# Optimization experiments

Measured on AMD Instinct MI355X. Metric: run time of the kernel, lower is better.

## Reference

```python
import jax, jax.numpy as jnp
import numpy as np

BS, C_IN, SEQ_LEN = 16, 321, 720
PRED_LEN, PATCH_LEN, STRIDE = 720, 24, 24
N_LAYERS, D_MODEL, N_HEADS, D_FF = 3, 128, 16, 256
SEQ_PN = (SEQ_LEN - PATCH_LEN) // STRIDE + 1   # 30
PRED_PN = (PRED_LEN + PATCH_LEN - 1) // PATCH_LEN  # 30
EPS = 1e-5


def layernorm(x, g, b):
    mu = x.mean(-1, keepdims=True)
    var = x.var(-1, keepdims=True)
    return (x - mu) * jax.lax.rsqrt(var + EPS) * g + b


def setup_inputs() -> dict:
    key = jax.random.key(0)
    ks = iter(jax.random.split(key, 32))
    w = lambda shape, s=0.02: jax.random.normal(next(ks), shape, jnp.float32) * s
    L = N_LAYERS
    return {
        "z": jax.random.normal(next(ks), (BS, C_IN, SEQ_LEN), jnp.float32),
        "W_P_w": w((D_MODEL, PATCH_LEN)), "W_P_b": jnp.zeros((D_MODEL,), jnp.float32),
        "PE": 0.04 * jax.random.uniform(next(ks), (SEQ_PN, D_MODEL), jnp.float32) - 0.02,
        "dummies": 0.5 * jax.random.normal(next(ks), (C_IN, PRED_PN, PATCH_LEN), jnp.float32),
        "Wq": w((L, D_MODEL, D_MODEL)), "bq": jnp.zeros((L, D_MODEL), jnp.float32),
        "Wk": w((L, D_MODEL, D_MODEL)), "bk": jnp.zeros((L, D_MODEL), jnp.float32),
        "Wv": w((L, D_MODEL, D_MODEL)), "bv": jnp.zeros((L, D_MODEL), jnp.float32),
        "Wo": w((L, D_MODEL, D_MODEL)), "bo": jnp.zeros((L, D_MODEL), jnp.float32),
        "g1": jnp.ones((L, D_MODEL), jnp.float32), "be1": jnp.zeros((L, D_MODEL), jnp.float32),
        "W1": w((L, D_FF, D_MODEL)), "b1": jnp.zeros((L, D_FF), jnp.float32),
        "W2": w((L, D_MODEL, D_FF // 2)), "b2": jnp.zeros((L, D_MODEL), jnp.float32),
        "g2": jnp.ones((L, D_MODEL), jnp.float32), "be2": jnp.zeros((L, D_MODEL), jnp.float32),
        "proj_w": w((PATCH_LEN, D_MODEL)), "proj_b": jnp.zeros((PATCH_LEN,), jnp.float32),
    }


def reference(z, W_P_w, W_P_b, PE, dummies, Wq, bq, Wk, bk, Wv, bv, Wo, bo,
              g1, be1, W1, b1, W2, b2, g2, be2, proj_w, proj_b):
    bs, c, _ = z.shape
    d_h = D_MODEL // N_HEADS
    scale = d_h ** -0.5
    # instance norm over time (unbiased=False var)
    mean = z.mean(2, keepdims=True)
    std = jnp.sqrt(z.var(2, keepdims=True) + EPS)
    zn = (z - mean) / std
    # unfold into patches: [bs, c, S, patch_len]
    idx = jnp.arange(SEQ_PN)[:, None] * STRIDE + jnp.arange(PATCH_LEN)[None, :]
    patches = zn[:, :, idx]
    x = jnp.einsum('bcsp,dp->bcsd', patches, W_P_w) + W_P_b + PE
    x = x.reshape(bs * c, SEQ_PN, D_MODEL)                       # seq tokens
    dum = jnp.einsum('cnp,dp->cnd', dummies, W_P_w) + W_P_b      # [c, Pn, d]
    pred = jnp.broadcast_to(dum[None], (bs, c, PRED_PN, D_MODEL)).reshape(bs * c, PRED_PN, D_MODEL)
    B = bs * c
    scores = None
    for i in range(N_LAYERS):
        q = (jnp.einsum('bpd,ed->bpe', pred, Wq[i]) + bq[i]).reshape(B, PRED_PN, N_HEADS, d_h)
        k = (jnp.einsum('bsd,ed->bse', x, Wk[i]) + bk[i]).reshape(B, SEQ_PN, N_HEADS, d_h)
        v = (jnp.einsum('bsd,ed->bse', x, Wv[i]) + bv[i]).reshape(B, SEQ_PN, N_HEADS, d_h)
        s = jnp.einsum('bphd,bshd->bphs', q, k) * scale
        if scores is not None:
            s = s + scores   # residual attention scores across layers
        scores = s
        attn = jax.nn.softmax(s, axis=-1)
        o = jnp.einsum('bphs,bshd->bphd', attn, v).reshape(B, PRED_PN, D_MODEL)
        o = jnp.einsum('bpd,ed->bpe', o, Wo[i]) + bo[i]
        pred = layernorm(pred + o, g1[i], be1[i])
        h = jnp.einsum('bpd,fd->bpf', pred, W1[i]) + b1[i]
        a, gate = jnp.split(h, 2, axis=-1)
        f = jnp.einsum('bpf,df->bpd', a * jax.nn.gelu(gate, approximate=False), W2[i]) + b2[i]
        pred = layernorm(pred + f, g2[i], be2[i])
    out = pred.reshape(bs, c, PRED_PN, D_MODEL)
    out = jnp.einsum('bcnd,pd->bcnp', out, proj_w) + proj_b
    out = out.reshape(bs, c, PRED_PN * PATCH_LEN)
    return out * std[:, :, 0:1] + mean[:, :, 0:1]
```

## Files before the change

### kernel.cpp

```cpp
#include <hip/hip_runtime.h>
#include <math.h>


typedef unsigned short u16;
typedef __attribute__((ext_vector_type(8))) short short8;
typedef __attribute__((ext_vector_type(4))) float floatx4;

#define ATTN_SCALE 0.35355339059327373f
#define SB 136
#define SF 132

#define MFMA_BF16 __builtin_amdgcn_mfma_f32_16x16x32_bf16

__device__ __forceinline__ u16 f2bf(float f){
  union{float f; unsigned u;} v; v.f=f;
  unsigned r = v.u + 0x7FFFu + ((v.u>>16)&1u);
  return (u16)(r>>16);
}
__device__ __forceinline__ float bf2f(u16 h){
  union{unsigned u; float f;} v; v.u = ((unsigned)h)<<16;
  return v.f;
}
__device__ __forceinline__ float gelu_f(float x){
  float u = x*(1.f + 0.044715f*x*x);
  float e = __expf(-1.5957691216057308f*u);
  return x/(1.f+e);
}

__device__ __forceinline__ short8 cvt8(const float* ap){
  floatx4 f0 = *(const floatx4*)ap;
  floatx4 f1 = *(const floatx4*)(ap+4);
  short8 a;
  a[0]=(short)f2bf(f0[0]); a[1]=(short)f2bf(f0[1]);
  a[2]=(short)f2bf(f0[2]); a[3]=(short)f2bf(f0[3]);
  a[4]=(short)f2bf(f1[0]); a[5]=(short)f2bf(f1[1]);
  a[6]=(short)f2bf(f1[2]); a[7]=(short)f2bf(f1[3]);
  return a;
}
__device__ __forceinline__ short8 loadB(const u16* p){ return *(const short8*)p; }
__device__ __forceinline__ short8 loadB(const float* p){ return cvt8(p); }

__device__ __forceinline__ void epi(u16* out, floatx4 acc, float bv, int rt, int qd, int col){
  #pragma unroll
  for (int r=0;r<4;++r){
    const int row = rt*16+qd*4+r;
    out[row*SB+col] = (row<30) ? f2bf(acc[r]+bv) : (u16)0;
  }
}

template<typename WT>
__device__ __forceinline__ void gemm2(const u16* A, const WT* __restrict__ W,
                                      const float* __restrict__ bias, u16* out,
                                      int wave, int lane){
  const int m=lane&15, qd=lane>>4, col=wave*16+m;
  floatx4 acc[2] = {{0.f,0.f,0.f,0.f},{0.f,0.f,0.f,0.f}};
  #pragma unroll
  for (int kt=0;kt<4;++kt){
    short8 b = loadB(W + col*128 + kt*32 + qd*8);
    #pragma unroll
    for (int rt=0;rt<2;++rt){
      short8 a = *(const short8*)(A + (rt*16+m)*SB + kt*32 + qd*8);
      acc[rt] = MFMA_BF16(a, b, acc[rt], 0,0,0);
    }
  }
  const float bv = bias[col];
  #pragma unroll
  for (int rt=0;rt<2;++rt) epi(out, acc[rt], bv, rt, qd, col);
}

template<typename WT>
__device__ __forceinline__ void gemm_kv(const u16* A,
                                        const WT* __restrict__ Wk, const float* __restrict__ bk,
                                        const WT* __restrict__ Wv, const float* __restrict__ bv_,
                                        u16* outk, u16* outv, int wave, int lane){
  const int m=lane&15, qd=lane>>4, col=wave*16+m;
  floatx4 acck[2] = {{0.f,0.f,0.f,0.f},{0.f,0.f,0.f,0.f}};
  floatx4 accv[2] = {{0.f,0.f,0.f,0.f},{0.f,0.f,0.f,0.f}};
  #pragma unroll
  for (int kt=0;kt<4;++kt){
    short8 bk8 = loadB(Wk + col*128 + kt*32 + qd*8);
    short8 bv8 = loadB(Wv + col*128 + kt*32 + qd*8);
    #pragma unroll
    for (int rt=0;rt<2;++rt){
      short8 a = *(const short8*)(A + (rt*16+m)*SB + kt*32 + qd*8);
      acck[rt] = MFMA_BF16(a, bk8, acck[rt], 0,0,0);
      accv[rt] = MFMA_BF16(a, bv8, accv[rt], 0,0,0);
    }
  }
  const float bkb = bk[col], bvb = bv_[col];
  #pragma unroll
  for (int rt=0;rt<2;++rt){
    epi(outk, acck[rt], bkb, rt, qd, col);
    epi(outv, accv[rt], bvb, rt, qd, col);
  }
}

template<typename WT>
__device__ __forceinline__ void gemm_h(const u16* A, const WT* __restrict__ W1,
                                       const float* __restrict__ b1, u16* out,
                                       int wave, int lane){
  const int m=lane&15, qd=lane>>4, col=wave*16+m;
  floatx4 acca[2] = {{0.f,0.f,0.f,0.f},{0.f,0.f,0.f,0.f}};
  floatx4 accg[2] = {{0.f,0.f,0.f,0.f},{0.f,0.f,0.f,0.f}};
  #pragma unroll
  for (int kt=0;kt<4;++kt){
    short8 ba = loadB(W1 + col*128 + kt*32 + qd*8);
    short8 bg = loadB(W1 + (128+col)*128 + kt*32 + qd*8);
    #pragma unroll
    for (int rt=0;rt<2;++rt){
      short8 a = *(const short8*)(A + (rt*16+m)*SB + kt*32 + qd*8);
      acca[rt] = MFMA_BF16(a, ba, acca[rt], 0,0,0);
      accg[rt] = MFMA_BF16(a, bg, accg[rt], 0,0,0);
    }
  }
  const float bab = b1[col], bgb = b1[128+col];
  #pragma unroll
  for (int rt=0;rt<2;++rt){
    #pragma unroll
    for (int r=0;r<4;++r){
      const int row = rt*16+qd*4+r;
      u16 res = 0;
      if (row<30){
        float a = acca[rt][r]+bab;
        float g = accg[rt][r]+bgb;
        res = f2bf(a * gelu_f(g));
      }
      out[row*SB+col] = res;
    }
  }
}

__device__ __forceinline__ void ln_res(float* pred, u16* predb, const u16* add,
                                       const float* __restrict__ g, const float* __restrict__ be,
                                       int wave, int lane){
  for (int rr=wave; rr<30; rr+=8){
    float* pr = pred + rr*SF;
    u16*  pbr = predb + rr*SB;
    const u16* ar = add + rr*SB;
    float v0 = pr[lane]    + bf2f(ar[lane]);
    float v1 = pr[lane+64] + bf2f(ar[lane+64]);
    float s = v0+v1, s2 = v0*v0+v1*v1;
    #pragma unroll
    for (int off=32; off>0; off>>=1){ s += __shfl_xor(s,off,64); s2 += __shfl_xor(s2,off,64); }
    float m = s*(1.f/128.f);
    float var = s2*(1.f/128.f) - m*m;
    float rstd = rsqrtf(var + 1e-5f);
    float o0 = (v0-m)*rstd*g[lane]    + be[lane];
    float o1 = (v1-m)*rstd*g[lane+64] + be[lane+64];
    pr[lane] = o0; pr[lane+64] = o1;
    pbr[lane] = f2bf(o0); pbr[lane+64] = f2bf(o1);
  }
}

__global__ void cvtw(const float* __restrict__ Wq, const float* __restrict__ Wk,
                     const float* __restrict__ Wv, const float* __restrict__ Wo,
                     const float* __restrict__ W1, const float* __restrict__ W2,
                     u16* __restrict__ ws){
  const int i = blockIdx.x*256 + threadIdx.x;
  float v;
  if      (i < 49152)  v = Wq[i];
  else if (i < 98304)  v = Wk[i-49152];
  else if (i < 147456) v = Wv[i-98304];
  else if (i < 196608) v = Wo[i-147456];
  else if (i < 294912) v = W1[i-196608];
  else                 v = W2[i-294912];
  ws[i] = f2bf(v);
}

template<typename WT>
__global__ void
__attribute__((amdgpu_flat_work_group_size(512,512), amdgpu_waves_per_eu(4)))
ts_fused(
  const float* __restrict__ z,    const float* __restrict__ WPw, const float* __restrict__ WPb,
  const float* __restrict__ PE,   const float* __restrict__ dums,
  const WT*    __restrict__ Wq_a, const float* __restrict__ bq_a,
  const WT*    __restrict__ Wk_a, const float* __restrict__ bk_a,
  const WT*    __restrict__ Wv_a, const float* __restrict__ bv_a,
  const WT*    __restrict__ Wo_a, const float* __restrict__ bo_a,
  const float* __restrict__ g1_a, const float* __restrict__ be1_a,
  const WT*    __restrict__ W1_a, const float* __restrict__ b1_a,
  const WT*    __restrict__ W2_a, const float* __restrict__ b2_a,
  const float* __restrict__ g2_a, const float* __restrict__ be2_a,
  const float* __restrict__ PJw,  const float* __restrict__ PJb,
  float* __restrict__ dout)
{
  __shared__ __align__(16) u16   x_s[32*SB];
  __shared__ __align__(16) u16   predb[32*SB];
  __shared__ __align__(16) float pred_s[30*SF];
  __shared__ __align__(16) u16   bufA[32*SB];
  __shared__ __align__(16) u16   bufB[32*SB];
  __shared__ __align__(16) u16   bufC[32*SB];
  __shared__ float redA[8], redB[8], stats[2];

  const int tid  = threadIdx.x;
  const int wave = tid >> 6;
  const int lane = tid & 63;
  const int bi   = blockIdx.x;
  const int c    = bi % 321;
  const float* zr = z + bi*720;

  float s=0.f, s2=0.f;
  for (int i=tid;i<720;i+=512){ float v=zr[i]; s+=v; s2+=v*v; }
  #pragma unroll
  for (int off=32; off>0; off>>=1){ s += __shfl_xor(s,off,64); s2 += __shfl_xor(s2,off,64); }
  if (lane==0){ redA[wave]=s; redB[wave]=s2; }
  __syncthreads();
  if (tid==0){
    float S=0.f,S2=0.f;
    #pragma unroll
    for (int w=0;w<8;++w){S+=redA[w];S2+=redB[w];}
    float mu = S*(1.f/720.f);
    float var = S2*(1.f/720.f) - mu*mu;
    stats[0]=mu; stats[1]=sqrtf(var+1e-5f);
  }
  __syncthreads();
  const float mu = stats[0], sd = stats[1], rsd = 1.f/sd;

  for (int i=tid;i<720;i+=512) bufA[i] = f2bf((zr[i]-mu)*rsd);
  __syncthreads();

  {
    const int m = lane&15, qd = lane>>4, col = wave*16+m;
    const short8 z8 = {0,0,0,0,0,0,0,0};
    short8 b = (qd<3) ? cvt8(WPw + col*24 + qd*8) : z8;
    const float bv = WPb[col];
    #pragma unroll
    for (int rt=0;rt<2;++rt){
      const int pm = rt*16+m;
      short8 ax = (pm<30 && qd<3) ? *(const short8*)(bufA + pm*24 + qd*8) : z8;
      short8 ap = (pm<30 && qd<3) ? cvt8(dums + c*720 + pm*24 + qd*8) : z8;
      floatx4 accx={0.f,0.f,0.f,0.f}, accp={0.f,0.f,0.f,0.f};
      accx = MFMA_BF16(ax,b,accx,0,0,0);
      accp = MFMA_BF16(ap,b,accp,0,0,0);
      #pragma unroll
      for (int r=0;r<4;++r){
        const int row = rt*16+qd*4+r;
        if (row<30){
          float pv = accp[r]+bv;
          x_s[row*SB+col]    = f2bf(accx[r]+bv+PE[row*128+col]);
          pred_s[row*SF+col] = pv;
          predb[row*SB+col]  = f2bf(pv);
        } else { x_s[row*SB+col]=0; predb[row*SB+col]=0; }
      }
    }
  }
  __syncthreads();

  float sc[30];
  #pragma unroll
  for (int i=0;i<30;++i) sc[i]=0.f;
  const int h = wave*2 + (lane>>5);
  const int p = lane & 31;

  for (int li=0; li<3; ++li){
    const WT* Wq = Wq_a + li*16384; const float* bq = bq_a + li*128;
    const WT* Wk = Wk_a + li*16384; const float* bk = bk_a + li*128;
    const WT* Wv = Wv_a + li*16384; const float* bv = bv_a + li*128;
    const WT* Wo = Wo_a + li*16384; const float* bo = bo_a + li*128;
    const WT* W1 = W1_a + li*32768; const float* b1 = b1_a + li*256;
    const WT* W2 = W2_a + li*16384; const float* b2 = b2_a + li*128;

    gemm2  (predb, Wq, bq, bufA, wave, lane);
    gemm_kv(x_s, Wk, bk, Wv, bv, bufB, bufC, wave, lane);
    __syncthreads();

    if (p < 30){
      short8 qq = *(const short8*)(bufA + p*SB + h*8);
      float qv[8];
      #pragma unroll
      for (int j=0;j<8;++j) qv[j]=bf2f((u16)qq[j]);
      #pragma unroll
      for (int si=0; si<30; ++si){
        short8 kk = *(const short8*)(bufB + si*SB + h*8);
        float d = 0.f;
        #pragma unroll
        for (int j=0;j<8;++j) d += qv[j]*bf2f((u16)kk[j]);
        sc[si] += d * ATTN_SCALE;
      }
      float mx = sc[0];
      #pragma unroll
      for (int si=1; si<30; ++si) mx = fmaxf(mx, sc[si]);
      float ssum = 0.f;
      float ov[8] = {0.f,0.f,0.f,0.f,0.f,0.f,0.f,0.f};
      #pragma unroll
      for (int si=0; si<30; ++si){
        float e = __expf(sc[si]-mx);
        ssum += e;
        short8 vv = *(const short8*)(bufC + si*SB + h*8);
        #pragma unroll
        for (int j=0;j<8;++j) ov[j] += e*bf2f((u16)vv[j]);
      }
      const float rn = 1.f/ssum;
      #pragma unroll
      for (int j=0;j<8;++j) bufA[p*SB+h*8+j] = f2bf(ov[j]*rn);
    }
    __syncthreads();

    gemm2(bufA, Wo, bo, bufB, wave, lane);
    __syncthreads();
    ln_res(pred_s, predb, bufB, g1_a+li*128, be1_a+li*128, wave, lane);
    __syncthreads();

    gemm_h(predb, W1, b1, bufC, wave, lane);
    __syncthreads();
    gemm2(bufC, W2, b2, bufB, wave, lane);
    __syncthreads();
    ln_res(pred_s, predb, bufB, g2_a+li*128, be2_a+li*128, wave, lane);
    __syncthreads();
  }

  {
    const int m = lane&15, qd = lane>>4;
    const short8 z8 = {0,0,0,0,0,0,0,0};
    float* orow = dout + bi*720;
    for (int t=wave; t<4; t+=8){
      const int rt=t>>1, ct=t&1;
      const int col = ct*16+m;
      floatx4 acc = {0.f,0.f,0.f,0.f};
      #pragma unroll
      for (int kt=0;kt<4;++kt){
        const int k0 = kt*32+qd*8;
        short8 a = *(const short8*)(predb + (rt*16+m)*SB + k0);
        short8 b = (col<24) ? cvt8(PJw + col*128 + k0) : z8;
        acc = MFMA_BF16(a,b,acc,0,0,0);
      }
      if (col<24){
        const float pb = PJb[col];
        #pragma unroll
        for (int r=0;r<4;++r){
          const int row = rt*16+qd*4+r;
          if (row<30) orow[row*24+col] = (acc[r]+pb)*sd + mu;
        }
      }
    }
  }
}

extern "C" void kernel_launch(void* const* d_in, const int* in_sizes, int n_in,
                              void* d_out, int out_size, void* d_ws, size_t ws_size,
                              hipStream_t stream) {
  (void)in_sizes; (void)n_in; (void)out_size;
  const float* z    = (const float*)d_in[0];
  const float* WPw  = (const float*)d_in[1];
  const float* WPb  = (const float*)d_in[2];
  const float* PE   = (const float*)d_in[3];
  const float* dums = (const float*)d_in[4];
  const float* Wq   = (const float*)d_in[5];
  const float* bq   = (const float*)d_in[6];
  const float* Wk   = (const float*)d_in[7];
  const float* bk   = (const float*)d_in[8];
  const float* Wv   = (const float*)d_in[9];
  const float* bv   = (const float*)d_in[10];
  const float* Wo   = (const float*)d_in[11];
  const float* bo   = (const float*)d_in[12];
  const float* g1   = (const float*)d_in[13];
  const float* be1  = (const float*)d_in[14];
  const float* W1   = (const float*)d_in[15];
  const float* b1   = (const float*)d_in[16];
  const float* W2   = (const float*)d_in[17];
  const float* b2   = (const float*)d_in[18];
  const float* g2   = (const float*)d_in[19];
  const float* be2  = (const float*)d_in[20];
  const float* PJw  = (const float*)d_in[21];
  const float* PJb  = (const float*)d_in[22];
  float* dout = (float*)d_out;

  const size_t need = (size_t)344064 * sizeof(u16);
  if (ws_size >= need){
    u16* ws = (u16*)d_ws;
    cvtw<<<dim3(1344), dim3(256), 0, stream>>>(Wq, Wk, Wv, Wo, W1, W2, ws);
    ts_fused<u16><<<dim3(5136), dim3(512), 0, stream>>>(
      z, WPw, WPb, PE, dums,
      ws,        bq, ws+49152,  bk, ws+98304, bv, ws+147456, bo,
      g1, be1, ws+196608, b1, ws+294912, b2, g2, be2, PJw, PJb, dout);
  } else {
    ts_fused<float><<<dim3(5136), dim3(512), 0, stream>>>(
      z, WPw, WPb, PE, dums,
      Wq, bq, Wk, bk, Wv, bv, Wo, bo,
      g1, be1, W1, b1, W2, b2, g2, be2, PJw, PJb, dout);
  }
}
```

Measured before the change: 1.029 ms.

## Halve block to 4 waves, double per-wave work, keep residual stream in registers

```diff
diff --git a/kernel.cpp b/kernel.cpp
--- a/kernel.cpp
+++ b/kernel.cpp
@@ -8,7 +8,7 @@
 
 #define ATTN_SCALE 0.35355339059327373f
 #define SB 136
-#define SF 132
+#define BUFSZ (30*SB)
 
 #define MFMA_BF16 __builtin_amdgcn_mfma_f32_16x16x32_bf16
 
@@ -44,7 +44,7 @@
   #pragma unroll
   for (int r=0;r<4;++r){
     const int row = rt*16+qd*4+r;
-    out[row*SB+col] = (row<30) ? f2bf(acc[r]+bv) : (u16)0;
+    if (row<30) out[row*SB+col] = f2bf(acc[r]+bv);
   }
 }
 
@@ -52,20 +52,27 @@
 __device__ __forceinline__ void gemm2(const u16* A, const WT* __restrict__ W,
                                       const float* __restrict__ bias, u16* out,
                                       int wave, int lane){
-  const int m=lane&15, qd=lane>>4, col=wave*16+m;
-  floatx4 acc[2] = {{0.f,0.f,0.f,0.f},{0.f,0.f,0.f,0.f}};
+  const int m=lane&15, qd=lane>>4, c0=wave*16+m;
+  floatx4 acc[2][2] = {{{0.f,0.f,0.f,0.f},{0.f,0.f,0.f,0.f}},
+                       {{0.f,0.f,0.f,0.f},{0.f,0.f,0.f,0.f}}};
   #pragma unroll
   for (int kt=0;kt<4;++kt){
-    short8 b = loadB(W + col*128 + kt*32 + qd*8);
+    short8 b0 = loadB(W + c0*128       + kt*32 + qd*8);
+    short8 b1 = loadB(W + (c0+64)*128  + kt*32 + qd*8);
     #pragma unroll
     for (int rt=0;rt<2;++rt){
       short8 a = *(const short8*)(A + (rt*16+m)*SB + kt*32 + qd*8);
-      acc[rt] = MFMA_BF16(a, b, acc[rt], 0,0,0);
-    }
-  }
-  const float bv = bias[col];
-  #pragma unroll
-  for (int rt=0;rt<2;++rt) epi(out, acc[rt], bv, rt, qd, col);
+      acc[0][rt] = MFMA_BF16(a, b0, acc[0][rt], 0,0,0);
+      acc[1][rt] = MFMA_BF16(a, b1, acc[1][rt], 0,0,0);
+    }
+  }
+  #pragma unroll
+  for (int ct=0;ct<2;++ct){
+    const int col = c0 + ct*64;
+    const float bv = bias[col];
+    #pragma unroll
+    for (int rt=0;rt<2;++rt) epi(out, acc[ct][rt], bv, rt, qd, col);
+  }
 }
 
 template<typename WT>
@@ -73,25 +80,35 @@
                                         const WT* __restrict__ Wk, const float* __restrict__ bk,
                                         const WT* __restrict__ Wv, const float* __restrict__ bv_,
                                         u16* outk, u16* outv, int wave, int lane){
-  const int m=lane&15, qd=lane>>4, col=wave*16+m;
-  floatx4 acck[2] = {{0.f,0.f,0.f,0.f},{0.f,0.f,0.f,0.f}};
-  floatx4 accv[2] = {{0.f,0.f,0.f,0.f},{0.f,0.f,0.f,0.f}};
+  const int m=lane&15, qd=lane>>4, c0=wave*16+m;
+  floatx4 acck[2][2] = {{{0.f,0.f,0.f,0.f},{0.f,0.f,0.f,0.f}},
+                        {{0.f,0.f,0.f,0.f},{0.f,0.f,0.f,0.f}}};
+  floatx4 accv[2][2] = {{{0.f,0.f,0.f,0.f},{0.f,0.f,0.f,0.f}},
+                        {{0.f,0.f,0.f,0.f},{0.f,0.f,0.f,0.f}}};
   #pragma unroll
   for (int kt=0;kt<4;++kt){
-    short8 bk8 = loadB(Wk + col*128 + kt*32 + qd*8);
-    short8 bv8 = loadB(Wv + col*128 + kt*32 + qd*8);
+    short8 bk0 = loadB(Wk + c0*128      + kt*32 + qd*8);
+    short8 bk1 = loadB(Wk + (c0+64)*128 + kt*32 + qd*8);
+    short8 bv0 = loadB(Wv + c0*128      + kt*32 + qd*8);
+    short8 bv1 = loadB(Wv + (c0+64)*128 + kt*32 + qd*8);
     #pragma unroll
     for (int rt=0;rt<2;++rt){
       short8 a = *(const short8*)(A + (rt*16+m)*SB + kt*32 + qd*8);
-      acck[rt] = MFMA_BF16(a, bk8, acck[rt], 0,0,0);
-      accv[rt] = MFMA_BF16(a, bv8, accv[rt], 0,0,0);
-    }
-  }
-  const float bkb = bk[col], bvb = bv_[col];
-  #pragma unroll
-  for (int rt=0;rt<2;++rt){
-    epi(outk, acck[rt], bkb, rt, qd, col);
-    epi(outv, accv[rt], bvb, rt, qd, col);
+      acck[0][rt] = MFMA_BF16(a, bk0, acck[0][rt], 0,0,0);
+      acck[1][rt] = MFMA_BF16(a, bk1, acck[1][rt], 0,0,0);
+      accv[0][rt] = MFMA_BF16(a, bv0, accv[0][rt], 0,0,0);
+      accv[1][rt] = MFMA_BF16(a, bv1, accv[1][rt], 0,0,0);
+    }
+  }
+  #pragma unroll
+  for (int ct=0;ct<2;++ct){
+    const int col = c0 + ct*64;
+    const float bkb = bk[col], bvb = bv_[col];
+    #pragma unroll
+    for (int rt=0;rt<2;++rt){
+      epi(outk, acck[ct][rt], bkb, rt, qd, col);
+      epi(outv, accv[ct][rt], bvb, rt, qd, col);
+    }
   }
 }
 
@@ -99,56 +116,67 @@
 __device__ __forceinline__ void gemm_h(const u16* A, const WT* __restrict__ W1,
                                        const float* __restrict__ b1, u16* out,
                                        int wave, int lane){
-  const int m=lane&15, qd=lane>>4, col=wave*16+m;
-  floatx4 acca[2] = {{0.f,0.f,0.f,0.f},{0.f,0.f,0.f,0.f}};
-  floatx4 accg[2] = {{0.f,0.f,0.f,0.f},{0.f,0.f,0.f,0.f}};
+  const int m=lane&15, qd=lane>>4, c0=wave*16+m;
+  floatx4 acca[2][2] = {{{0.f,0.f,0.f,0.f},{0.f,0.f,0.f,0.f}},
+                        {{0.f,0.f,0.f,0.f},{0.f,0.f,0.f,0.f}}};
+  floatx4 accg[2][2] = {{{0.f,0.f,0.f,0.f},{0.f,0.f,0.f,0.f}},
+                        {{0.f,0.f,0.f,0.f},{0.f,0.f,0.f,0.f}}};
   #pragma unroll
   for (int kt=0;kt<4;++kt){
-    short8 ba = loadB(W1 + col*128 + kt*32 + qd*8);
-    short8 bg = loadB(W1 + (128+col)*128 + kt*32 + qd*8);
+    short8 ba0 = loadB(W1 + c0*128        + kt*32 + qd*8);
+    short8 ba1 = loadB(W1 + (c0+64)*128   + kt*32 + qd*8);
+    short8 bg0 = loadB(W1 + (c0+128)*128  + kt*32 + qd*8);
+    short8 bg1 = loadB(W1 + (c0+192)*128  + kt*32 + qd*8);
     #pragma unroll
     for (int rt=0;rt<2;++rt){
       short8 a = *(const short8*)(A + (rt*16+m)*SB + kt*32 + qd*8);
-      acca[rt] = MFMA_BF16(a, ba, acca[rt], 0,0,0);
-      accg[rt] = MFMA_BF16(a, bg, accg[rt], 0,0,0);
-    }
-  }
-  const float bab = b1[col], bgb = b1[128+col];
-  #pragma unroll
-  for (int rt=0;rt<2;++rt){
-    #pragma unroll
-    for (int r=0;r<4;++r){
-      const int row = rt*16+qd*4+r;
-      u16 res = 0;
-      if (row<30){
-        float a = acca[rt][r]+bab;
-        float g = accg[rt][r]+bgb;
-        res = f2bf(a * gelu_f(g));
+      acca[0][rt] = MFMA_BF16(a, ba0, acca[0][rt], 0,0,0);
+      acca[1][rt] = MFMA_BF16(a, ba1, acca[1][rt], 0,0,0);
+      accg[0][rt] = MFMA_BF16(a, bg0, accg[0][rt], 0,0,0);
+      accg[1][rt] = MFMA_BF16(a, bg1, accg[1][rt], 0,0,0);
+    }
+  }
+  #pragma unroll
+  for (int ct=0;ct<2;++ct){
+    const int ca = c0 + ct*64;
+    const float bab = b1[ca], bgb = b1[128+ca];
+    #pragma unroll
+    for (int rt=0;rt<2;++rt){
+      #pragma unroll
+      for (int r=0;r<4;++r){
+        const int row = rt*16+qd*4+r;
+        if (row<30){
+          float a = acca[ct][rt][r]+bab;
+          float g = accg[ct][rt][r]+bgb;
+          out[row*SB+ca] = f2bf(a * gelu_f(g));
+        }
       }
-      out[row*SB+col] = res;
-    }
-  }
-}
-
-__device__ __forceinline__ void ln_res(float* pred, u16* predb, const u16* add,
-                                       const float* __restrict__ g, const float* __restrict__ be,
-                                       int wave, int lane){
-  for (int rr=wave; rr<30; rr+=8){
-    float* pr = pred + rr*SF;
-    u16*  pbr = predb + rr*SB;
-    const u16* ar = add + rr*SB;
-    float v0 = pr[lane]    + bf2f(ar[lane]);
-    float v1 = pr[lane+64] + bf2f(ar[lane+64]);
-    float s = v0+v1, s2 = v0*v0+v1*v1;
-    #pragma unroll
-    for (int off=32; off>0; off>>=1){ s += __shfl_xor(s,off,64); s2 += __shfl_xor(s2,off,64); }
-    float m = s*(1.f/128.f);
-    float var = s2*(1.f/128.f) - m*m;
-    float rstd = rsqrtf(var + 1e-5f);
-    float o0 = (v0-m)*rstd*g[lane]    + be[lane];
-    float o1 = (v1-m)*rstd*g[lane+64] + be[lane+64];
-    pr[lane] = o0; pr[lane+64] = o1;
-    pbr[lane] = f2bf(o0); pbr[lane+64] = f2bf(o1);
+    }
+  }
+}
+
+__device__ __forceinline__ void ln_res_reg(float (&p0)[8], float (&p1)[8],
+                                           const u16* add, u16* predb,
+                                           const float* __restrict__ g, const float* __restrict__ be,
+                                           int wave, int lane){
+  #pragma unroll
+  for (int idx=0; idx<8; ++idx){
+    const int row = wave + idx*4;
+    if (row < 30){
+      float v0 = p0[idx] + bf2f(add[row*SB+lane]);
+      float v1 = p1[idx] + bf2f(add[row*SB+lane+64]);
+      float s = v0+v1, s2 = v0*v0+v1*v1;
+      #pragma unroll
+      for (int off=32; off>0; off>>=1){ s += __shfl_xor(s,off,64); s2 += __shfl_xor(s2,off,64); }
+      float m = s*(1.f/128.f);
+      float var = s2*(1.f/128.f) - m*m;
+      float rstd = rsqrtf(var + 1e-5f);
+      float o0 = (v0-m)*rstd*g[lane]    + be[lane];
+      float o1 = (v1-m)*rstd*g[lane+64] + be[lane+64];
+      p0[idx] = o0; p1[idx] = o1;
+      predb[row*SB+lane]    = f2bf(o0);
+      predb[row*SB+lane+64] = f2bf(o1);
+    }
   }
 }
 
@@ -169,7 +197,7 @@
 
 template<typename WT>
 __global__ void
-__attribute__((amdgpu_flat_work_group_size(512,512), amdgpu_waves_per_eu(4)))
+__attribute__((amdgpu_flat_work_group_size(256,256), amdgpu_waves_per_eu(3)))
 ts_fused(
   const float* __restrict__ z,    const float* __restrict__ WPw, const float* __restrict__ WPb,
   const float* __restrict__ PE,   const float* __restrict__ dums,
@@ -184,13 +212,14 @@
   const float* __restrict__ PJw,  const float* __restrict__ PJb,
   float* __restrict__ dout)
 {
-  __shared__ __align__(16) u16   x_s[32*SB];
-  __shared__ __align__(16) u16   predb[32*SB];
-  __shared__ __align__(16) float pred_s[30*SF];
-  __shared__ __align__(16) u16   bufA[32*SB];
-  __shared__ __align__(16) u16   bufB[32*SB];
-  __shared__ __align__(16) u16   bufC[32*SB];
-  __shared__ float redA[8], redB[8], stats[2];
+  __shared__ __align__(16) u16 SH[5*BUFSZ + 2*SB];
+  __shared__ float redA[4], redB[4], stats[2];
+
+  u16* const x_s   = SH;
+  u16* const predb = SH + BUFSZ;
+  u16* const bufA  = SH + 2*BUFSZ;
+  u16* const bufB  = SH + 3*BUFSZ;
+  u16* const bufC  = SH + 4*BUFSZ;
 
   const int tid  = threadIdx.x;
   const int wave = tid >> 6;
@@ -200,7 +229,7 @@
   const float* zr = z + bi*720;
 
   float s=0.f, s2=0.f;
-  for (int i=tid;i<720;i+=512){ float v=zr[i]; s+=v; s2+=v*v; }
+  for (int i=tid;i<720;i+=256){ float v=zr[i]; s+=v; s2+=v*v; }
   #pragma unroll
   for (int off=32; off>0; off>>=1){ s += __shfl_xor(s,off,64); s2 += __shfl_xor(s2,off,64); }
   if (lane==0){ redA[wave]=s; redB[wave]=s2; }
@@ -208,7 +237,7 @@
   if (tid==0){
     float S=0.f,S2=0.f;
     #pragma unroll
-    for (int w=0;w<8;++w){S+=redA[w];S2+=redB[w];}
+    for (int w=0;w<4;++w){S+=redA[w];S2+=redB[w];}
     float mu = S*(1.f/720.f);
     float var = S2*(1.f/720.f) - mu*mu;
     stats[0]=mu; stats[1]=sqrtf(var+1e-5f);
@@ -216,39 +245,58 @@
   __syncthreads();
   const float mu = stats[0], sd = stats[1], rsd = 1.f/sd;
 
-  for (int i=tid;i<720;i+=512) bufA[i] = f2bf((zr[i]-mu)*rsd);
+  for (int i=tid;i<720;i+=256) bufC[i] = f2bf((zr[i]-mu)*rsd);
   __syncthreads();
 
   {
-    const int m = lane&15, qd = lane>>4, col = wave*16+m;
+    float* pf = (float*)(SH + 2*BUFSZ);
+    const int m = lane&15, qd = lane>>4;
     const short8 z8 = {0,0,0,0,0,0,0,0};
-    short8 b = (qd<3) ? cvt8(WPw + col*24 + qd*8) : z8;
-    const float bv = WPb[col];
-    #pragma unroll
-    for (int rt=0;rt<2;++rt){
-      const int pm = rt*16+m;
-      short8 ax = (pm<30 && qd<3) ? *(const short8*)(bufA + pm*24 + qd*8) : z8;
-      short8 ap = (pm<30 && qd<3) ? cvt8(dums + c*720 + pm*24 + qd*8) : z8;
-      floatx4 accx={0.f,0.f,0.f,0.f}, accp={0.f,0.f,0.f,0.f};
-      accx = MFMA_BF16(ax,b,accx,0,0,0);
-      accp = MFMA_BF16(ap,b,accp,0,0,0);
+    #pragma unroll
+    for (int ct=0;ct<2;++ct){
+      const int col = ct*64 + wave*16 + m;
+      short8 b = (qd<3) ? cvt8(WPw + col*24 + qd*8) : z8;
+      const float bv = WPb[col];
       #pragma unroll
-      for (int r=0;r<4;++r){
-        const int row = rt*16+qd*4+r;
-        if (row<30){
-          float pv = accp[r]+bv;
-          x_s[row*SB+col]    = f2bf(accx[r]+bv+PE[row*128+col]);
-          pred_s[row*SF+col] = pv;
-          predb[row*SB+col]  = f2bf(pv);
-        } else { x_s[row*SB+col]=0; predb[row*SB+col]=0; }
+      for (int rt=0;rt<2;++rt){
+        const int pm = rt*16+m;
+        short8 ax = (pm<30 && qd<3) ? *(const short8*)(bufC + pm*24 + qd*8) : z8;
+        short8 ap = (pm<30 && qd<3) ? cvt8(dums + c*720 + pm*24 + qd*8) : z8;
+        floatx4 accx={0.f,0.f,0.f,0.f}, accp={0.f,0.f,0.f,0.f};
+        accx = MFMA_BF16(ax,b,accx,0,0,0);
+        accp = MFMA_BF16(ap,b,accp,0,0,0);
+        #pragma unroll
+        for (int r=0;r<4;++r){
+          const int row = rt*16+qd*4+r;
+          if (row<30){
+            float pv = accp[r]+bv;
+            x_s[row*SB+col]   = f2bf(accx[r]+bv+PE[row*128+col]);
+            pf[row*128+col]   = pv;
+            predb[row*SB+col] = f2bf(pv);
+          }
+        }
       }
     }
   }
   __syncthreads();
 
-  float sc[30];
-  #pragma unroll
-  for (int i=0;i<30;++i) sc[i]=0.f;
+  float p0[8], p1[8];
+  {
+    const float* pf = (const float*)(SH + 2*BUFSZ);
+    #pragma unroll
+    for (int idx=0; idx<8; ++idx){
+      const int row = wave + idx*4;
+      p0[idx] = (row<30) ? pf[row*128+lane]    : 0.f;
+      p1[idx] = (row<30) ? pf[row*128+lane+64] : 0.f;
+    }
+  }
+  __syncthreads();
+
+  float sc[2][30];
+  #pragma unroll
+  for (int s2i=0;s2i<2;++s2i)
+    #pragma unroll
+    for (int i=0;i<30;++i) sc[s2i][i]=0.f;
   const int h = wave*2 + (lane>>5);
   const int p = lane & 31;
 
@@ -265,72 +313,74 @@
     __syncthreads();
 
     if (p < 30){
-      short8 qq = *(const short8*)(bufA + p*SB + h*8);
-      float qv[8];
       #pragma unroll
-      for (int j=0;j<8;++j) qv[j]=bf2f((u16)qq[j]);
-      #pragma unroll
-      for (int si=0; si<30; ++si){
-        short8 kk = *(const short8*)(bufB + si*SB + h*8);
-        float d = 0.f;
-        #pragma unroll
-        for (int j=0;j<8;++j) d += qv[j]*bf2f((u16)kk[j]);
-        sc[si] += d * ATTN_SCALE;
+      for (int s2i=0;s2i<2;++s2i){
+        const int he = h + s2i*8;
+        short8 qq = *(const short8*)(bufA + p*SB + he*8);
+        float qv[8];
+        #pragma unroll
+        for (int j=0;j<8;++j) qv[j]=bf2f((u16)qq[j]);
+        #pragma unroll
+        for (int si=0; si<30; ++si){
+          short8 kk = *(const short8*)(bufB + si*SB + he*8);
+          float d = 0.f;
+          #pragma unroll
+          for (int j=0;j<8;++j) d += qv[j]*bf2f((u16)kk[j]);
+          sc[s2i][si] += d * ATTN_SCALE;
+        }
+        float mx = sc[s2i][0];
+        #pragma unroll
+        for (int si=1; si<30; ++si) mx = fmaxf(mx, sc[s2i][si]);
+        float ssum = 0.f;
+        float ov[8] = {0.f,0.f,0.f,0.f,0.f,0.f,0.f,0.f};
+        #pragma unroll
+        for (int si=0; si<30; ++si){
+          float e = __expf(sc[s2i][si]-mx);
+          ssum += e;
+          short8 vv = *(const short8*)(bufC + si*SB + he*8);
+          #pragma unroll
+          for (int j=0;j<8;++j) ov[j] += e*bf2f((u16)vv[j]);
+        }
+        const float rn = 1.f/ssum;
+        #pragma unroll
+        for (int j=0;j<8;++j) bufA[p*SB+he*8+j] = f2bf(ov[j]*rn);
       }
-      float mx = sc[0];
-      #pragma unroll
-      for (int si=1; si<30; ++si) mx = fmaxf(mx, sc[si]);
-      float ssum = 0.f;
-      float ov[8] = {0.f,0.f,0.f,0.f,0.f,0.f,0.f,0.f};
-      #pragma unroll
-      for (int si=0; si<30; ++si){
-        float e = __expf(sc[si]-mx);
-        ssum += e;
-        short8 vv = *(const short8*)(bufC + si*SB + h*8);
-        #pragma unroll
-        for (int j=0;j<8;++j) ov[j] += e*bf2f((u16)vv[j]);
-      }
-      const float rn = 1.f/ssum;
-      #pragma unroll
-      for (int j=0;j<8;++j) bufA[p*SB+h*8+j] = f2bf(ov[j]*rn);
     }
     __syncthreads();
 
     gemm2(bufA, Wo, bo, bufB, wave, lane);
     __syncthreads();
-    ln_res(pred_s, predb, bufB, g1_a+li*128, be1_a+li*128, wave, lane);
+    ln_res_reg(p0, p1, bufB, predb, g1_a+li*128, be1_a+li*128, wave, lane);
     __syncthreads();
 
     gemm_h(predb, W1, b1, bufC, wave, lane);
     __syncthreads();
     gemm2(bufC, W2, b2, bufB, wave, lane);
     __syncthreads();
-    ln_res(pred_s, predb, bufB, g2_a+li*128, be2_a+li*128, wave, lane);
+    ln_res_reg(p0, p1, bufB, predb, g2_a+li*128, be2_a+li*128, wave, lane);
     __syncthreads();
   }
 
   {
     const int m = lane&15, qd = lane>>4;
     const short8 z8 = {0,0,0,0,0,0,0,0};
+    const int rt = wave>>1, ct = wave&1;
+    const int col = ct*16+m;
     float* orow = dout + bi*720;
-    for (int t=wave; t<4; t+=8){
-      const int rt=t>>1, ct=t&1;
-      const int col = ct*16+m;
-      floatx4 acc = {0.f,0.f,0.f,0.f};
+    floatx4 acc = {0.f,0.f,0.f,0.f};
+    #pragma unroll
+    for (int kt=0;kt<4;++kt){
+      const int k0 = kt*32+qd*8;
+      short8 a = *(const short8*)(predb + (rt*16+m)*SB + k0);
+      short8 b = (col<24) ? cvt8(PJw + col*128 + k0) : z8;
+      acc = MFMA_BF16(a,b,acc,0,0,0);
+    }
+    if (col<24){
+      const float pb = PJb[col];
       #pragma unroll
-      for (int kt=0;kt<4;++kt){
-        const int k0 = kt*32+qd*8;
-        short8 a = *(const short8*)(predb + (rt*16+m)*SB + k0);
-        short8 b = (col<24) ? cvt8(PJw + col*128 + k0) : z8;
-        acc = MFMA_BF16(a,b,acc,0,0,0);
-      }
-      if (col<24){
-        const float pb = PJb[col];
-        #pragma unroll
-        for (int r=0;r<4;++r){
-          const int row = rt*16+qd*4+r;
-          if (row<30) orow[row*24+col] = (acc[r]+pb)*sd + mu;
-        }
+      for (int r=0;r<4;++r){
+        const int row = rt*16+qd*4+r;
+        if (row<30) orow[row*24+col] = (acc[r]+pb)*sd + mu;
       }
     }
   }
@@ -369,12 +419,12 @@
   if (ws_size >= need){
     u16* ws = (u16*)d_ws;
     cvtw<<<dim3(1344), dim3(256), 0, stream>>>(Wq, Wk, Wv, Wo, W1, W2, ws);
-    ts_fused<u16><<<dim3(5136), dim3(512), 0, stream>>>(
+    ts_fused<u16><<<dim3(5136), dim3(256), 0, stream>>>(
       z, WPw, WPb, PE, dums,
       ws,        bq, ws+49152,  bk, ws+98304, bv, ws+147456, bo,
       g1, be1, ws+196608, b1, ws+294912, b2, g2, be2, PJw, PJb, dout);
   } else {
-    ts_fused<float><<<dim3(5136), dim3(512), 0, stream>>>(
+    ts_fused<float><<<dim3(5136), dim3(256), 0, stream>>>(
       z, WPw, WPb, PE, dums,
       Wq, bq, Wk, bk, Wv, bv, Wo, bo,
       g1, be1, W1, b1, W2, b2, g2, be2, PJw, PJb, dout);
```

New measurement: 1.151 ms. 11.9% more time.
